# Performance work log

Measured on AMD Instinct MI355X. Metric: run time of the kernel, lower is better.

Reference implementation:

```python
import math
import jax, jax.numpy as jnp
import numpy as np

N, DIN, DOUT = 32768, 1024, 1024
C = 1.0            # ball curvature c (k = -c)
MIN_NORM = 1e-15
EPS_PROJ = 4e-3    # geoopt float32 boundary eps


def _safe_norm(x):
    # sqrt of clipped sum-of-squares: finite value and finite grad at 0
    return jnp.sqrt(jnp.clip(jnp.sum(x * x, axis=-1, keepdims=True), MIN_NORM))


def _artanh(u):
    return jnp.arctanh(jnp.clip(u, -1.0 + 1e-5, 1.0 - 1e-5))


def _project(x, c):
    norm = _safe_norm(x)
    maxnorm = (1.0 - EPS_PROJ) / jnp.sqrt(c)
    return jnp.where(norm > maxnorm, x / norm * maxnorm, x)


def _mobius_matvec(W, x, c):
    sqc = jnp.sqrt(c)
    x_norm = _safe_norm(x)                       # [N,1]
    mx = x @ W.T                                 # [N,DOUT]
    mx_norm = _safe_norm(mx)                     # [N,1]
    res = jnp.tanh(mx_norm / x_norm * _artanh(sqc * x_norm)) * mx / (mx_norm * sqc)
    zero = jnp.all(mx == 0, axis=-1, keepdims=True)
    return jnp.where(zero, jnp.zeros((), x.dtype), res)


def _expmap0(u, c):
    sqc = jnp.sqrt(c)
    u_norm = _safe_norm(u)
    return jnp.tanh(sqc * u_norm) * u / (sqc * u_norm)


def _mobius_add(x, y, c):
    x2 = jnp.sum(x * x, axis=-1, keepdims=True)
    y2 = jnp.sum(y * y, axis=-1, keepdims=True)
    xy = jnp.sum(x * y, axis=-1, keepdims=True)
    num = (1.0 + 2.0 * c * xy + c * y2) * x + (1.0 - c * x2) * y
    denom = 1.0 + 2.0 * c * xy + c * c * x2 * y2
    return num / jnp.clip(denom, MIN_NORM)


def setup_inputs() -> dict:
    key = jax.random.key(0)
    kx, kw, kb = jax.random.split(key, 3)
    x = jax.random.normal(kx, (N, DIN), jnp.float32)
    # place points strictly inside the unit Poincare ball
    x = x / (jnp.linalg.norm(x, axis=-1, keepdims=True) + 1.0) * 0.7
    limit = math.sqrt(2.0) * math.sqrt(6.0 / (DIN + DOUT))  # xavier_uniform gain=sqrt(2)
    weight = jax.random.uniform(kw, (DOUT, DIN), jnp.float32, -limit, limit)
    bias = 0.01 * jax.random.normal(kb, (DOUT,), jnp.float32)
    return {"x": x, "weight": weight, "bias": bias}


def reference(x, weight, bias) -> jnp.ndarray:
    c = jnp.float32(C)
    res = _mobius_matvec(weight, x, c)           # dropout=0 / eval: weight used as-is
    res = _project(res, c)
    hyp_bias = _project(_expmap0(bias[None, :], c), c)
    res = _project(_mobius_add(res, hyp_bias, c), c)
    return res
```

## Files before the change

### kernel.cpp

```cpp
#include <hip/hip_runtime.h>
#include <hip/hip_bf16.h>
#include <cmath>

#define NROWS 32768
#define DIN   1024
#define DOUT  1024
#define BM    64
#define BK    32
#define NKT   (DIN / BK)
#define MAXNORM 0.996f
#define XPAD  40

typedef __attribute__((ext_vector_type(8))) __bf16 bf16x8;
typedef __attribute__((ext_vector_type(4))) float  f32x4;

__device__ __forceinline__ void gload16(const void* g, void* l) {
    __builtin_amdgcn_global_load_lds(
        (const __attribute__((address_space(1))) void*)g,
        (__attribute__((address_space(3))) void*)l, 16, 0, 0);
}

__device__ __forceinline__ unsigned pack2bf(float a, float b) {
    union { unsigned u; __bf16 h[2]; } p;
    p.h[0] = (__bf16)a; p.h[1] = (__bf16)b;
    return p.u;
}

#define WAITBAR(N) do {                                                   \
    asm volatile("s_waitcnt vmcnt(" #N ") lgkmcnt(0)" ::: "memory");      \
    __builtin_amdgcn_s_barrier();                                         \
    __builtin_amdgcn_sched_barrier(0);                                    \
} while (0)

__global__ void conv_w_kernel(const float* __restrict__ Wf, __bf16* __restrict__ Wb) {
    int cid = blockIdx.x * blockDim.x + threadIdx.x;
    int q  = cid & 3;
    int r  = (cid >> 2) & 15;
    int g2 = (cid >> 6) & 31;
    int h  = (cid >> 11) & 1;
    int kt = cid >> 12;
    int n  = ((g2 << 1) + h) * 16 + r;
    int k0 = kt * BK + ((q ^ ((r >> 1) & 3)) << 3);
    const float* src = Wf + (size_t)n * DIN + k0;
    f32x4 v0 = *(const f32x4*)src;
    f32x4 v1 = *(const f32x4*)(src + 4);
    uint4 o;
    o.x = pack2bf(v0[0], v0[1]); o.y = pack2bf(v0[2], v0[3]);
    o.z = pack2bf(v1[0], v1[1]); o.w = pack2bf(v1[2], v1[3]);
    *(uint4*)((char*)Wb + (size_t)cid * 16) = o;
}

__global__ __launch_bounds__(512, 2) void hyp_kernel_pipe(
    const float* __restrict__ X,
    const __bf16* __restrict__ Wb,
    const float* __restrict__ bias,
    float* __restrict__ out)
{
    __shared__ __align__(16) __bf16 WtA[2][512 * BK];
    __shared__ __align__(16) __bf16 WtB[2][512 * BK];
    __shared__ __align__(16) __bf16 Xt[2][BM * XPAD];
    __shared__ float hbs[DOUT];
    __shared__ float redq[BM][8];
    __shared__ float redd[BM][8];
    __shared__ float xsqs[BM];
    __shared__ float fco[BM][2];
    __shared__ float bred[8];

    const int tid  = threadIdx.x;
    const int lane = tid & 63;
    const int wid  = tid >> 6;
    const int l15  = lane & 15;
    const int l4   = lane >> 4;
    const int row0 = blockIdx.x * BM;

    const int xr = tid >> 3;
    const int xk = (tid & 7) * 4;
    const float* xp = X + (size_t)(row0 + xr) * DIN + xk;
    float xsq = 0.f;

    f32x4 acc[4][8];
    #pragma unroll
    for (int m = 0; m < 4; m++)
        #pragma unroll
        for (int nt = 0; nt < 8; nt++)
            acc[m][nt] = (f32x4){0.f, 0.f, 0.f, 0.f};

    auto wsrc = [&](int kt, int h) -> const char* {
        return (const char*)Wb + (((size_t)kt * 2 + h) << 15);
    };
    auto issueHalf = [&](const char* g, __bf16* lds) {
        #pragma unroll
        for (int j = 0; j < 4; j++) {
            int c = (j << 9) + tid;
            gload16(g + (size_t)c * 16,
                    (char*)lds + (((j << 9) + (wid << 6)) << 4));
        }
    };

    f32x4 xv;
    auto xload  = [&](int kt) { xv = *(const f32x4*)(xp + kt * BK); };
    auto xstage = [&](int dstbuf) {
        xsq += xv[0]*xv[0] + xv[1]*xv[1] + xv[2]*xv[2] + xv[3]*xv[3];
        uint2 pk;
        pk.x = pack2bf(xv[0], xv[1]);
        pk.y = pack2bf(xv[2], xv[3]);
        *(uint2*)((char*)(&Xt[dstbuf][0]) + xr * (XPAD * 2) + xk * 2) = pk;
    };

    bf16x8 afr[4];
    auto cmpA = [&](int buf) {
        const char* xb = (const char*)(&Xt[buf][0]);
        const char* wb = (const char*)(&WtA[buf][0]);
        #pragma unroll
        for (int m = 0; m < 4; m++)
            afr[m] = *(const bf16x8*)(xb + ((m << 4) + l15) * (XPAD * 2) + (l4 << 4));
        bf16x8 b[4];
        #pragma unroll
        for (int i = 0; i < 4; i++) {
            int g2 = (wid << 2) + i;
            b[i] = *(const bf16x8*)(wb + (((g2 << 6) + (l15 << 2) + (l4 ^ ((l15 >> 1) & 3))) << 4));
        }
        __builtin_amdgcn_s_setprio(1);
        #pragma unroll
        for (int i = 0; i < 4; i++)
            #pragma unroll
            for (int m = 0; m < 4; m++)
                acc[m][i * 2] = __builtin_amdgcn_mfma_f32_16x16x32_bf16(afr[m], b[i], acc[m][i * 2], 0, 0, 0);
        __builtin_amdgcn_s_setprio(0);
    };
    auto cmpB = [&](int buf) {
        const char* wb = (const char*)(&WtB[buf][0]);
        bf16x8 b[4];
        #pragma unroll
        for (int i = 0; i < 4; i++) {
            int g2 = (wid << 2) + i;
            b[i] = *(const bf16x8*)(wb + (((g2 << 6) + (l15 << 2) + (l4 ^ ((l15 >> 1) & 3))) << 4));
        }
        __builtin_amdgcn_s_setprio(1);
        #pragma unroll
        for (int i = 0; i < 4; i++)
            #pragma unroll
            for (int m = 0; m < 4; m++)
                acc[m][i * 2 + 1] = __builtin_amdgcn_mfma_f32_16x16x32_bf16(afr[m], b[i], acc[m][i * 2 + 1], 0, 0, 0);
        __builtin_amdgcn_s_setprio(0);
    };

    issueHalf(wsrc(0, 0), &WtA[0][0]);
    issueHalf(wsrc(0, 1), &WtB[0][0]);
    xload(0);

    float b0 = bias[tid], b1 = bias[tid + 512];
    float bs = b0 * b0 + b1 * b1;
    #pragma unroll
    for (int m = 1; m < 64; m <<= 1) bs += __shfl_xor(bs, m);
    if (lane == 0) bred[wid] = bs;
    __syncthreads();
    float tot = 0.f;
    #pragma unroll
    for (int i = 0; i < 8; i++) tot += bred[i];
    const float bnorm = sqrtf(fmaxf(tot, 1e-15f));
    const float bth   = tanhf(bnorm);
    float sc0 = bth / bnorm;
    float hn  = bth;
    if (hn > MAXNORM) { sc0 *= MAXNORM / hn; hn = MAXNORM; }
    hbs[tid]       = sc0 * b0;
    hbs[tid + 512] = sc0 * b1;
    const float y2c = hn * hn;
    __syncthreads();

    float hv[8];
    #pragma unroll
    for (int nt = 0; nt < 8; nt++) hv[nt] = hbs[(wid << 7) + (nt << 4) + l15];

    xstage(0);
    xload(1);

    for (int kt = 0; kt < 30; kt += 2) {
        issueHalf(wsrc(kt + 1, 0), &WtA[1][0]); WAITBAR(9); cmpA(0);
        xstage(1); xload(kt + 2);
        issueHalf(wsrc(kt + 1, 1), &WtB[1][0]); WAITBAR(9); cmpB(0);

        issueHalf(wsrc(kt + 2, 0), &WtA[0][0]); WAITBAR(9); cmpA(1);
        xstage(0); xload(kt + 3);
        issueHalf(wsrc(kt + 2, 1), &WtB[0][0]); WAITBAR(9); cmpB(1);
    }
    issueHalf(wsrc(31, 0), &WtA[1][0]); WAITBAR(9); cmpA(0);
    xstage(1);
    issueHalf(wsrc(31, 1), &WtB[1][0]); WAITBAR(8); cmpB(0);
    WAITBAR(4); cmpA(1);
    WAITBAR(0); cmpB(1);

    float xs = xsq;
    #pragma unroll
    for (int m = 1; m < 8; m <<= 1) xs += __shfl_xor(xs, m);
    if ((tid & 7) == 0) xsqs[xr] = xs;

    #pragma unroll
    for (int m = 0; m < 4; m++) {
        #pragma unroll
        for (int r = 0; r < 4; r++) {
            float s = 0.f, d = 0.f;
            #pragma unroll
            for (int nt = 0; nt < 8; nt++) {
                float v = acc[m][nt][r];
                s += v * v;
                d += v * hv[nt];
            }
            #pragma unroll
            for (int mm = 1; mm < 16; mm <<= 1) {
                s += __shfl_xor(s, mm);
                d += __shfl_xor(d, mm);
            }
            if (l15 == 0) {
                int rl = (m << 4) + (l4 << 2) + r;
                redq[rl][wid] = s;
                redd[rl][wid] = d;
            }
        }
    }
    __syncthreads();

    if (tid < BM) {
        int r = tid;
        float sq = 0.f, dt = 0.f;
        #pragma unroll
        for (int w = 0; w < 8; w++) { sq += redq[r][w]; dt += redd[r][w]; }
        float sx     = xsqs[r];
        float xnorm  = sqrtf(fmaxf(sx, 1e-15f));
        float mxnorm = sqrtf(fmaxf(sq, 1e-15f));
        float u  = fminf(xnorm, 1.f - 1e-5f);
        float tv = tanhf(mxnorm / xnorm * atanhf(u));
        float rn = fminf(tv, MAXNORM);
        float s  = rn / mxnorm;
        float xy = s * dt;
        float x2 = rn * rn;
        float Am = 1.f + 2.f * xy + y2c;
        float Bm = 1.f - x2;
        float Dm = fmaxf(1.f + 2.f * xy + x2 * y2c, 1e-15f);
        float g1 = Am * s / Dm;
        float g2 = Bm / Dm;
        float osq   = g1 * g1 * sq + 2.f * g1 * g2 * dt + g2 * g2 * y2c;
        float onorm = sqrtf(fmaxf(osq, 1e-15f));
        float psc   = onorm > MAXNORM ? MAXNORM / onorm : 1.f;
        fco[r][0] = g1 * psc;
        fco[r][1] = g2 * psc;
    }
    __syncthreads();

    #pragma unroll
    for (int m = 0; m < 4; m++) {
        #pragma unroll
        for (int r = 0; r < 4; r++) {
            int rl = (m << 4) + (l4 << 2) + r;
            float F1 = fco[rl][0], F2 = fco[rl][1];
            float* orow = out + (size_t)(row0 + rl) * DOUT + (wid << 7);
            #pragma unroll
            for (int nt = 0; nt < 8; nt++)
                orow[(nt << 4) + l15] = F1 * acc[m][nt][r] + F2 * hv[nt];
        }
    }
}

__global__ __launch_bounds__(512, 2) void hyp_kernel_basic(
    const float* __restrict__ X,
    const float* __restrict__ Wf,
    const float* __restrict__ bias,
    float* __restrict__ out)
{
    __shared__ __align__(16) __bf16 Wt[2][DOUT * BK];
    __shared__ __align__(16) __bf16 Xt[2][BM * XPAD];
    __shared__ float hbs[DOUT];
    __shared__ float redq[BM][8];
    __shared__ float redd[BM][8];
    __shared__ float xsqs[BM];
    __shared__ float fco[BM][2];
    __shared__ float bred[8];

    const int tid  = threadIdx.x;
    const int lane = tid & 63;
    const int wid  = tid >> 6;
    const int l15  = lane & 15;
    const int l4   = lane >> 4;
    const int row0 = blockIdx.x * BM;
    const int xr = tid >> 3;
    const int xk = (tid & 7) * 4;
    const float* xp = X + (size_t)(row0 + xr) * DIN + xk;
    float xsq = 0.f;

    f32x4 acc[4][8];
    #pragma unroll
    for (int m = 0; m < 4; m++)
        #pragma unroll
        for (int nt = 0; nt < 8; nt++)
            acc[m][nt] = (f32x4){0.f, 0.f, 0.f, 0.f};

    auto STAGE = [&](int buf, int kt) {
        if (kt < NKT) {
            #pragma unroll
            for (int j = 0; j < 8; j++) {
                int c = (j << 9) + tid;
                int q = c & 3, n = c >> 2;
                int k0 = kt * BK + ((q ^ ((n >> 1) & 3)) << 3);
                const float* src = Wf + (size_t)n * DIN + k0;
                f32x4 v0 = *(const f32x4*)src;
                f32x4 v1 = *(const f32x4*)(src + 4);
                uint4 o;
                o.x = pack2bf(v0[0], v0[1]); o.y = pack2bf(v0[2], v0[3]);
                o.z = pack2bf(v1[0], v1[1]); o.w = pack2bf(v1[2], v1[3]);
                *(uint4*)((char*)(&Wt[buf][0]) + c * 16) = o;
            }
            f32x4 xv = *(const f32x4*)(xp + kt * BK);
            xsq += xv[0]*xv[0] + xv[1]*xv[1] + xv[2]*xv[2] + xv[3]*xv[3];
            uint2 pk;
            pk.x = pack2bf(xv[0], xv[1]);
            pk.y = pack2bf(xv[2], xv[3]);
            *(uint2*)((char*)(&Xt[buf][0]) + xr * (XPAD * 2) + xk * 2) = pk;
        }
    };

    STAGE(0, 0);

    float b0 = bias[tid], b1 = bias[tid + 512];
    float bs = b0 * b0 + b1 * b1;
    #pragma unroll
    for (int m = 1; m < 64; m <<= 1) bs += __shfl_xor(bs, m);
    if (lane == 0) bred[wid] = bs;
    __syncthreads();
    float tot = 0.f;
    #pragma unroll
    for (int i = 0; i < 8; i++) tot += bred[i];
    const float bnorm = sqrtf(fmaxf(tot, 1e-15f));
    const float bth   = tanhf(bnorm);
    float sc0 = bth / bnorm;
    float hn  = bth;
    if (hn > MAXNORM) { sc0 *= MAXNORM / hn; hn = MAXNORM; }
    hbs[tid]       = sc0 * b0;
    hbs[tid + 512] = sc0 * b1;
    const float y2c = hn * hn;
    __syncthreads();

    float hv[8];
    #pragma unroll
    for (int nt = 0; nt < 8; nt++) hv[nt] = hbs[(wid << 7) + (nt << 4) + l15];

    int cur = 0;
    for (int kt = 0; kt < NKT; kt++) {
        STAGE(cur ^ 1, kt + 1);
        const char* xb = (const char*)(&Xt[cur][0]);
        const char* wb = (const char*)(&Wt[cur][0]);
        bf16x8 a[4], b[8];
        #pragma unroll
        for (int m = 0; m < 4; m++)
            a[m] = *(const bf16x8*)(xb + ((m << 4) + l15) * (XPAD * 2) + (l4 << 4));
        #pragma unroll
        for (int nt = 0; nt < 8; nt++) {
            int n = (wid << 7) + (nt << 4) + l15;
            b[nt] = *(const bf16x8*)(wb + n * 64 + ((l4 ^ ((n >> 1) & 3)) << 4));
        }
        #pragma unroll
        for (int m = 0; m < 4; m++)
            #pragma unroll
            for (int nt = 0; nt < 8; nt++)
                acc[m][nt] = __builtin_amdgcn_mfma_f32_16x16x32_bf16(a[m], b[nt], acc[m][nt], 0, 0, 0);
        __syncthreads();
        cur ^= 1;
    }

    float xs = xsq;
    #pragma unroll
    for (int m = 1; m < 8; m <<= 1) xs += __shfl_xor(xs, m);
    if ((tid & 7) == 0) xsqs[xr] = xs;

    #pragma unroll
    for (int m = 0; m < 4; m++) {
        #pragma unroll
        for (int r = 0; r < 4; r++) {
            float s = 0.f, d = 0.f;
            #pragma unroll
            for (int nt = 0; nt < 8; nt++) {
                float v = acc[m][nt][r];
                s += v * v;
                d += v * hv[nt];
            }
            #pragma unroll
            for (int mm = 1; mm < 16; mm <<= 1) {
                s += __shfl_xor(s, mm);
                d += __shfl_xor(d, mm);
            }
            if (l15 == 0) {
                int rl = (m << 4) + (l4 << 2) + r;
                redq[rl][wid] = s;
                redd[rl][wid] = d;
            }
        }
    }
    __syncthreads();

    if (tid < BM) {
        int r = tid;
        float sq = 0.f, dt = 0.f;
        #pragma unroll
        for (int w = 0; w < 8; w++) { sq += redq[r][w]; dt += redd[r][w]; }
        float sx     = xsqs[r];
        float xnorm  = sqrtf(fmaxf(sx, 1e-15f));
        float mxnorm = sqrtf(fmaxf(sq, 1e-15f));
        float u  = fminf(xnorm, 1.f - 1e-5f);
        float tv = tanhf(mxnorm / xnorm * atanhf(u));
        float rn = fminf(tv, MAXNORM);
        float s  = rn / mxnorm;
        float xy = s * dt;
        float x2 = rn * rn;
        float Am = 1.f + 2.f * xy + y2c;
        float Bm = 1.f - x2;
        float Dm = fmaxf(1.f + 2.f * xy + x2 * y2c, 1e-15f);
        float g1 = Am * s / Dm;
        float g2 = Bm / Dm;
        float osq   = g1 * g1 * sq + 2.f * g1 * g2 * dt + g2 * g2 * y2c;
        float onorm = sqrtf(fmaxf(osq, 1e-15f));
        float psc   = onorm > MAXNORM ? MAXNORM / onorm : 1.f;
        fco[r][0] = g1 * psc;
        fco[r][1] = g2 * psc;
    }
    __syncthreads();

    #pragma unroll
    for (int m = 0; m < 4; m++) {
        #pragma unroll
        for (int r = 0; r < 4; r++) {
            int rl = (m << 4) + (l4 << 2) + r;
            float F1 = fco[rl][0], F2 = fco[rl][1];
            float* orow = out + (size_t)(row0 + rl) * DOUT + (wid << 7);
            #pragma unroll
            for (int nt = 0; nt < 8; nt++)
                orow[(nt << 4) + l15] = F1 * acc[m][nt][r] + F2 * hv[nt];
        }
    }
}

extern "C" void kernel_launch(void* const* d_in, const int* in_sizes, int n_in,
                              void* d_out, int out_size, void* d_ws, size_t ws_size,
                              hipStream_t stream) {
    const float* X    = (const float*)d_in[0];
    const float* W    = (const float*)d_in[1];
    const float* bias = (const float*)d_in[2];
    float* out = (float*)d_out;

    const size_t wb_bytes = (size_t)DOUT * DIN * 2;
    if (ws_size >= wb_bytes) {
        __bf16* Wb = (__bf16*)d_ws;
        conv_w_kernel<<<dim3(512), dim3(256), 0, stream>>>(W, Wb);
        hyp_kernel_pipe<<<dim3(NROWS / BM), dim3(512), 0, stream>>>(X, Wb, bias, out);
    } else {
        hyp_kernel_basic<<<dim3(NROWS / BM), dim3(512), 0, stream>>>(X, W, bias, out);
    }
}
```

Before: 121.7 us.

## Load weight fragments directly into registers from pre-laid-out global buffer

Replaces the LDS-staged async weight pipeline with a 1024-thread kernel where each wave loads its bf16 weight MFMA fragments straight from global memory into registers, prefetched one k-step ahead, and only X goes through a triple-buffered LDS tile. The weight conversion kernel is rewritten to emit a fragment-major layout so each lane's loads are contiguous. This drops the LDS traffic and bank pressure for W and frees shared memory. In exchange, every wave re-reads W from L2 with only a one-step prefetch, so global latency may be exposed. Per-wave output width shrinks from 128 to 64 columns, which lowers reuse of the X fragments.

After: 112.1 us. 7.8% less time.

```diff
diff --git a/kernel.cpp b/kernel.cpp
--- a/kernel.cpp
+++ b/kernel.cpp
@@ -14,50 +14,213 @@
 typedef __attribute__((ext_vector_type(8))) __bf16 bf16x8;
 typedef __attribute__((ext_vector_type(4))) float  f32x4;
 
-__device__ __forceinline__ void gload16(const void* g, void* l) {
-    __builtin_amdgcn_global_load_lds(
-        (const __attribute__((address_space(1))) void*)g,
-        (__attribute__((address_space(3))) void*)l, 16, 0, 0);
-}
-
 __device__ __forceinline__ unsigned pack2bf(float a, float b) {
     union { unsigned u; __bf16 h[2]; } p;
     p.h[0] = (__bf16)a; p.h[1] = (__bf16)b;
     return p.u;
 }
 
-#define WAITBAR(N) do {                                                   \
-    asm volatile("s_waitcnt vmcnt(" #N ") lgkmcnt(0)" ::: "memory");      \
-    __builtin_amdgcn_s_barrier();                                         \
-    __builtin_amdgcn_sched_barrier(0);                                    \
-} while (0)
-
 __global__ void conv_w_kernel(const float* __restrict__ Wf, __bf16* __restrict__ Wb) {
-    int cid = blockIdx.x * blockDim.x + threadIdx.x;
-    int q  = cid & 3;
-    int r  = (cid >> 2) & 15;
-    int g2 = (cid >> 6) & 31;
-    int h  = (cid >> 11) & 1;
-    int kt = cid >> 12;
-    int n  = ((g2 << 1) + h) * 16 + r;
-    int k0 = kt * BK + ((q ^ ((r >> 1) & 3)) << 3);
+    int c  = blockIdx.x * blockDim.x + threadIdx.x;
+    int l  = c & 63;
+    int j  = (c >> 6) & 63;
+    int kt = c >> 12;
+    int n  = j * 16 + (l & 15);
+    int k0 = kt * 32 + (l >> 4) * 8;
     const float* src = Wf + (size_t)n * DIN + k0;
     f32x4 v0 = *(const f32x4*)src;
     f32x4 v1 = *(const f32x4*)(src + 4);
     uint4 o;
     o.x = pack2bf(v0[0], v0[1]); o.y = pack2bf(v0[2], v0[3]);
     o.z = pack2bf(v1[0], v1[1]); o.w = pack2bf(v1[2], v1[3]);
-    *(uint4*)((char*)Wb + (size_t)cid * 16) = o;
+    *(uint4*)((char*)Wb + (size_t)c * 16) = o;
 }
 
-__global__ __launch_bounds__(512, 2) void hyp_kernel_pipe(
+__global__ __launch_bounds__(1024) void hyp_kernel_reg(
     const float* __restrict__ X,
     const __bf16* __restrict__ Wb,
     const float* __restrict__ bias,
     float* __restrict__ out)
 {
-    __shared__ __align__(16) __bf16 WtA[2][512 * BK];
-    __shared__ __align__(16) __bf16 WtB[2][512 * BK];
+    __shared__ __align__(16) __bf16 Xt[3][BM * XPAD];
+    __shared__ float hbs[DOUT];
+    __shared__ float xsqs[BM];
+    __shared__ float fco[BM][2];
+    __shared__ float bred[16];
+
+    const int tid  = threadIdx.x;
+    const int lane = tid & 63;
+    const int wid  = tid >> 6;
+    const int l15  = lane & 15;
+    const int l4   = lane >> 4;
+    const int row0 = blockIdx.x * BM;
+
+    const int xr = tid >> 4;
+    const int xk = (tid & 15) * 2;
+    const float* xp = X + (size_t)(row0 + xr) * DIN + xk;
+    float xsq = 0.f;
+
+    const __bf16* wp = Wb + ((size_t)(wid * 4) * 64 + lane) * 8;
+
+    f32x4 acc[4][4];
+    #pragma unroll
+    for (int m = 0; m < 4; m++)
+        #pragma unroll
+        for (int n = 0; n < 4; n++)
+            acc[m][n] = (f32x4){0.f, 0.f, 0.f, 0.f};
+
+    float2 xw = *(const float2*)xp;
+    float2 xf = *(const float2*)(xp + BK);
+    bf16x8 bfr[4];
+    #pragma unroll
+    for (int i = 0; i < 4; i++) bfr[i] = *(const bf16x8*)(wp + i * 512);
+
+    float bv = bias[tid];
+    float bs = bv * bv;
+    #pragma unroll
+    for (int m = 1; m < 64; m <<= 1) bs += __shfl_xor(bs, m);
+    if (lane == 0) bred[wid] = bs;
+    __syncthreads();
+    float tot = 0.f;
+    #pragma unroll
+    for (int i = 0; i < 16; i++) tot += bred[i];
+    const float bnorm = sqrtf(fmaxf(tot, 1e-15f));
+    const float bth   = tanhf(bnorm);
+    float sc0 = bth / bnorm;
+    float hn  = bth;
+    if (hn > MAXNORM) { sc0 *= MAXNORM / hn; hn = MAXNORM; }
+    hbs[tid] = sc0 * bv;
+    const float y2c = hn * hn;
+
+    xsq += xw.x * xw.x + xw.y * xw.y;
+    *(unsigned*)((char*)(&Xt[0][0]) + xr * (XPAD * 2) + xk * 2) = pack2bf(xw.x, xw.y);
+    xw = xf;
+    xf = *(const float2*)(xp + 2 * BK);
+
+    int br = 0, bw = 1;
+    for (int kt = 0; kt < NKT; kt++) {
+        if (kt + 1 < NKT) {
+            xsq += xw.x * xw.x + xw.y * xw.y;
+            *(unsigned*)((char*)(&Xt[bw][0]) + xr * (XPAD * 2) + xk * 2) = pack2bf(xw.x, xw.y);
+        }
+        xw = xf;
+        int xt = kt + 3 < NKT ? kt + 3 : NKT - 1;
+        xf = *(const float2*)(xp + (size_t)xt * BK);
+
+        asm volatile("s_waitcnt lgkmcnt(0)" ::: "memory");
+        __builtin_amdgcn_s_barrier();
+        __builtin_amdgcn_sched_barrier(0);
+
+        bf16x8 a[4];
+        const char* xb = (const char*)(&Xt[br][0]);
+        #pragma unroll
+        for (int m = 0; m < 4; m++)
+            a[m] = *(const bf16x8*)(xb + ((m << 4) + l15) * (XPAD * 2) + (l4 << 4));
+
+        __builtin_amdgcn_s_setprio(1);
+        #pragma unroll
+        for (int n = 0; n < 4; n++)
+            #pragma unroll
+            for (int m = 0; m < 4; m++)
+                acc[m][n] = __builtin_amdgcn_mfma_f32_16x16x32_bf16(a[m], bfr[n], acc[m][n], 0, 0, 0);
+        __builtin_amdgcn_s_setprio(0);
+
+        int ktb = kt + 1 < NKT ? kt + 1 : NKT - 1;
+        const __bf16* wkp = wp + (size_t)ktb * 32768;
+        #pragma unroll
+        for (int i = 0; i < 4; i++) bfr[i] = *(const bf16x8*)(wkp + i * 512);
+
+        br = br + 1 == 3 ? 0 : br + 1;
+        bw = bw + 1 == 3 ? 0 : bw + 1;
+    }
+
+    __syncthreads();
+
+    float* redq = (float*)(&Xt[0][0]);
+    float* redd = redq + BM * 16;
+
+    float xs = xsq;
+    #pragma unroll
+    for (int m = 1; m < 16; m <<= 1) xs += __shfl_xor(xs, m);
+    if (l15 == 0) xsqs[xr] = xs;
+
+    float hv[4];
+    #pragma unroll
+    for (int n = 0; n < 4; n++) hv[n] = hbs[(wid << 6) + (n << 4) + l15];
+
+    #pragma unroll
+    for (int m = 0; m < 4; m++) {
+        #pragma unroll
+        for (int r = 0; r < 4; r++) {
+            float s = 0.f, d = 0.f;
+            #pragma unroll
+            for (int n = 0; n < 4; n++) {
+                float v = acc[m][n][r];
+                s += v * v;
+                d += v * hv[n];
+            }
+            #pragma unroll
+            for (int mm = 1; mm < 16; mm <<= 1) {
+                s += __shfl_xor(s, mm);
+                d += __shfl_xor(d, mm);
+            }
+            if (l15 == 0) {
+                int rl = (m << 4) + (l4 << 2) + r;
+                redq[rl * 16 + wid] = s;
+                redd[rl * 16 + wid] = d;
+            }
+        }
+    }
+    __syncthreads();
+
+    if (tid < BM) {
+        int r = tid;
+        float sq = 0.f, dt = 0.f;
+        #pragma unroll
+        for (int w = 0; w < 16; w++) { sq += redq[r * 16 + w]; dt += redd[r * 16 + w]; }
+        float sx     = xsqs[r];
+        float xnorm  = sqrtf(fmaxf(sx, 1e-15f));
+        float mxnorm = sqrtf(fmaxf(sq, 1e-15f));
+        float u  = fminf(xnorm, 1.f - 1e-5f);
+        float tv = tanhf(mxnorm / xnorm * atanhf(u));
+        float rn = fminf(tv, MAXNORM);
+        float s  = rn / mxnorm;
+        float xy = s * dt;
+        float x2 = rn * rn;
+        float Am = 1.f + 2.f * xy + y2c;
+        float Bm = 1.f - x2;
+        float Dm = fmaxf(1.f + 2.f * xy + x2 * y2c, 1e-15f);
+        float g1 = Am * s / Dm;
+        float g2 = Bm / Dm;
+        float osq   = g1 * g1 * sq + 2.f * g1 * g2 * dt + g2 * g2 * y2c;
+        float onorm = sqrtf(fmaxf(osq, 1e-15f));
+        float psc   = onorm > MAXNORM ? MAXNORM / onorm : 1.f;
+        fco[r][0] = g1 * psc;
+        fco[r][1] = g2 * psc;
+    }
+    __syncthreads();
+
+    #pragma unroll
+    for (int m = 0; m < 4; m++) {
+        #pragma unroll
+        for (int r = 0; r < 4; r++) {
+            int rl = (m << 4) + (l4 << 2) + r;
+            float F1 = fco[rl][0], F2 = fco[rl][1];
+            float* orow = out + (size_t)(row0 + rl) * DOUT + (wid << 6);
+            #pragma unroll
+            for (int n = 0; n < 4; n++)
+                orow[(n << 4) + l15] = F1 * acc[m][n][r] + F2 * hv[n];
+        }
+    }
+}
+
+__global__ __launch_bounds__(512, 2) void hyp_kernel_basic(
+    const float* __restrict__ X,
+    const float* __restrict__ Wf,
+    const float* __restrict__ bias,
+    float* __restrict__ out)
+{
+    __shared__ __align__(16) __bf16 Wt[2][DOUT * BK];
     __shared__ __align__(16) __bf16 Xt[2][BM * XPAD];
     __shared__ float hbs[DOUT];
     __shared__ float redq[BM][8];
@@ -72,7 +235,6 @@
     const int l15  = lane & 15;
     const int l4   = lane >> 4;
     const int row0 = blockIdx.x * BM;
-
     const int xr = tid >> 3;
     const int xk = (tid & 7) * 4;
     const float* xp = X + (size_t)(row0 + xr) * DIN + xk;
@@ -85,69 +247,31 @@
         for (int nt = 0; nt < 8; nt++)
             acc[m][nt] = (f32x4){0.f, 0.f, 0.f, 0.f};
 
-    auto wsrc = [&](int kt, int h) -> const char* {
-        return (const char*)Wb + (((size_t)kt * 2 + h) << 15);
+    auto STAGE = [&](int buf, int kt) {
+        if (kt < NKT) {
+            #pragma unroll
+            for (int j = 0; j < 8; j++) {
+                int c = (j << 9) + tid;
+                int q = c & 3, n = c >> 2;
+                int k0 = kt * BK + ((q ^ ((n >> 1) & 3)) << 3);
+                const float* src = Wf + (size_t)n * DIN + k0;
+                f32x4 v0 = *(const f32x4*)src;
+                f32x4 v1 = *(const f32x4*)(src + 4);
+                uint4 o;
+                o.x = pack2bf(v0[0], v0[1]); o.y = pack2bf(v0[2], v0[3]);
+                o.z = pack2bf(v1[0], v1[1]); o.w = pack2bf(v1[2], v1[3]);
+                *(uint4*)((char*)(&Wt[buf][0]) + c * 16) = o;
+            }
+            f32x4 xv = *(const f32x4*)(xp + kt * BK);
+            xsq += xv[0]*xv[0] + xv[1]*xv[1] + xv[2]*xv[2] + xv[3]*xv[3];
+            uint2 pk;
+            pk.x = pack2bf(xv[0], xv[1]);
+            pk.y = pack2bf(xv[2], xv[3]);
+            *(uint2*)((char*)(&Xt[buf][0]) + xr * (XPAD * 2) + xk * 2) = pk;
+        }
     };
-    auto issueHalf = [&](const char* g, __bf16* lds) {
-        #pragma unroll
-        for (int j = 0; j < 4; j++) {
-            int c = (j << 9) + tid;
-            gload16(g + (size_t)c * 16,
-                    (char*)lds + (((j << 9) + (wid << 6)) << 4));
-        }
-    };
-
-    f32x4 xv;
-    auto xload  = [&](int kt) { xv = *(const f32x4*)(xp + kt * BK); };
-    auto xstage = [&](int dstbuf) {
-        xsq += xv[0]*xv[0] + xv[1]*xv[1] + xv[2]*xv[2] + xv[3]*xv[3];
-        uint2 pk;
-        pk.x = pack2bf(xv[0], xv[1]);
-        pk.y = pack2bf(xv[2], xv[3]);
-        *(uint2*)((char*)(&Xt[dstbuf][0]) + xr * (XPAD * 2) + xk * 2) = pk;
-    };
-
-    bf16x8 afr[4];
-    auto cmpA = [&](int buf) {
-        const char* xb = (const char*)(&Xt[buf][0]);
-        const char* wb = (const char*)(&WtA[buf][0]);
-        #pragma unroll
-        for (int m = 0; m < 4; m++)
-            afr[m] = *(const bf16x8*)(xb + ((m << 4) + l15) * (XPAD * 2) + (l4 << 4));
-        bf16x8 b[4];
-        #pragma unroll
-        for (int i = 0; i < 4; i++) {
-            int g2 = (wid << 2) + i;
-            b[i] = *(const bf16x8*)(wb + (((g2 << 6) + (l15 << 2) + (l4 ^ ((l15 >> 1) & 3))) << 4));
-        }
-        __builtin_amdgcn_s_setprio(1);
-        #pragma unroll
-        for (int i = 0; i < 4; i++)
-            #pragma unroll
-            for (int m = 0; m < 4; m++)
-                acc[m][i * 2] = __builtin_amdgcn_mfma_f32_16x16x32_bf16(afr[m], b[i], acc[m][i * 2], 0, 0, 0);
-        __builtin_amdgcn_s_setprio(0);
-    };
-    auto cmpB = [&](int buf) {
-        const char* wb = (const char*)(&WtB[buf][0]);
-        bf16x8 b[4];
-        #pragma unroll
-        for (int i = 0; i < 4; i++) {
-            int g2 = (wid << 2) + i;
-            b[i] = *(const bf16x8*)(wb + (((g2 << 6) + (l15 << 2) + (l4 ^ ((l15 >> 1) & 3))) << 4));
-        }
-        __builtin_amdgcn_s_setprio(1);
-        #pragma unroll
-        for (int i = 0; i < 4; i++)
-            #pragma unroll
-            for (int m = 0; m < 4; m++)
-                acc[m][i * 2 + 1] = __builtin_amdgcn_mfma_f32_16x16x32_bf16(afr[m], b[i], acc[m][i * 2 + 1], 0, 0, 0);
-        __builtin_amdgcn_s_setprio(0);
-    };
-
-    issueHalf(wsrc(0, 0), &WtA[0][0]);
-    issueHalf(wsrc(0, 1), &WtB[0][0]);
-    xload(0);
+
+    STAGE(0, 0);
 
     float b0 = bias[tid], b1 = bias[tid + 512];
     float bs = b0 * b0 + b1 * b1;
@@ -172,23 +296,28 @@
     #pragma unroll
     for (int nt = 0; nt < 8; nt++) hv[nt] = hbs[(wid << 7) + (nt << 4) + l15];
 
-    xstage(0);
-    xload(1);
-
-    for (int kt = 0; kt < 30; kt += 2) {
-        issueHalf(wsrc(kt + 1, 0), &WtA[1][0]); WAITBAR(9); cmpA(0);
-        xstage(1); xload(kt + 2);
-        issueHalf(wsrc(kt + 1, 1), &WtB[1][0]); WAITBAR(9); cmpB(0);
-
-        issueHalf(wsrc(kt + 2, 0), &WtA[0][0]); WAITBAR(9); cmpA(1);
-        xstage(0); xload(kt + 3);
-        issueHalf(wsrc(kt + 2, 1), &WtB[0][0]); WAITBAR(9); cmpB(1);
-    }
-    issueHalf(wsrc(31, 0), &WtA[1][0]); WAITBAR(9); cmpA(0);
-    xstage(1);
-    issueHalf(wsrc(31, 1), &WtB[1][0]); WAITBAR(8); cmpB(0);
-    WAITBAR(4); cmpA(1);
-    WAITBAR(0); cmpB(1);
+    int cur = 0;
+    for (int kt = 0; kt < NKT; kt++) {
+        STAGE(cur ^ 1, kt + 1);
+        const char* xb = (const char*)(&Xt[cur][0]);
+        const char* wb = (const char*)(&Wt[cur][0]);
+        bf16x8 a[4], b[8];
+        #pragma unroll
+        for (int m = 0; m < 4; m++)
+            a[m] = *(const bf16x8*)(xb + ((m << 4) + l15) * (XPAD * 2) + (l4 << 4));
+        #pragma unroll
+        for (int nt = 0; nt < 8; nt++) {
+            int n = (wid << 7) + (nt << 4) + l15;
+            b[nt] = *(const bf16x8*)(wb + n * 64 + ((l4 ^ ((n >> 1) & 3)) << 4));
+        }
+        #pragma unroll
+        for (int m = 0; m < 4; m++)
+            #pragma unroll
+            for (int nt = 0; nt < 8; nt++)
+                acc[m][nt] = __builtin_amdgcn_mfma_f32_16x16x32_bf16(a[m], b[nt], acc[m][nt], 0, 0, 0);
+        __syncthreads();
+        cur ^= 1;
+    }
 
     float xs = xsq;
     #pragma unroll
@@ -261,182 +390,6 @@
     }
 }
 
-__global__ __launch_bounds__(512, 2) void hyp_kernel_basic(
-    const float* __restrict__ X,
-    const float* __restrict__ Wf,
-    const float* __restrict__ bias,
-    float* __restrict__ out)
-{
-    __shared__ __align__(16) __bf16 Wt[2][DOUT * BK];
-    __shared__ __align__(16) __bf16 Xt[2][BM * XPAD];
-    __shared__ float hbs[DOUT];
-    __shared__ float redq[BM][8];
-    __shared__ float redd[BM][8];
-    __shared__ float xsqs[BM];
-    __shared__ float fco[BM][2];
-    __shared__ float bred[8];
-
-    const int tid  = threadIdx.x;
-    const int lane = tid & 63;
-    const int wid  = tid >> 6;
-    const int l15  = lane & 15;
-    const int l4   = lane >> 4;
-    const int row0 = blockIdx.x * BM;
-    const int xr = tid >> 3;
-    const int xk = (tid & 7) * 4;
-    const float* xp = X + (size_t)(row0 + xr) * DIN + xk;
-    float xsq = 0.f;
-
-    f32x4 acc[4][8];
-    #pragma unroll
-    for (int m = 0; m < 4; m++)
-        #pragma unroll
-        for (int nt = 0; nt < 8; nt++)
-            acc[m][nt] = (f32x4){0.f, 0.f, 0.f, 0.f};
-
-    auto STAGE = [&](int buf, int kt) {
-        if (kt < NKT) {
-            #pragma unroll
-            for (int j = 0; j < 8; j++) {
-                int c = (j << 9) + tid;
-                int q = c & 3, n = c >> 2;
-                int k0 = kt * BK + ((q ^ ((n >> 1) & 3)) << 3);
-                const float* src = Wf + (size_t)n * DIN + k0;
-                f32x4 v0 = *(const f32x4*)src;
-                f32x4 v1 = *(const f32x4*)(src + 4);
-                uint4 o;
-                o.x = pack2bf(v0[0], v0[1]); o.y = pack2bf(v0[2], v0[3]);
-                o.z = pack2bf(v1[0], v1[1]); o.w = pack2bf(v1[2], v1[3]);
-                *(uint4*)((char*)(&Wt[buf][0]) + c * 16) = o;
-            }
-            f32x4 xv = *(const f32x4*)(xp + kt * BK);
-            xsq += xv[0]*xv[0] + xv[1]*xv[1] + xv[2]*xv[2] + xv[3]*xv[3];
-            uint2 pk;
-            pk.x = pack2bf(xv[0], xv[1]);
-            pk.y = pack2bf(xv[2], xv[3]);
-            *(uint2*)((char*)(&Xt[buf][0]) + xr * (XPAD * 2) + xk * 2) = pk;
-        }
-    };
-
-    STAGE(0, 0);
-
-    float b0 = bias[tid], b1 = bias[tid + 512];
-    float bs = b0 * b0 + b1 * b1;
-    #pragma unroll
-    for (int m = 1; m < 64; m <<= 1) bs += __shfl_xor(bs, m);
-    if (lane == 0) bred[wid] = bs;
-    __syncthreads();
-    float tot = 0.f;
-    #pragma unroll
-    for (int i = 0; i < 8; i++) tot += bred[i];
-    const float bnorm = sqrtf(fmaxf(tot, 1e-15f));
-    const float bth   = tanhf(bnorm);
-    float sc0 = bth / bnorm;
-    float hn  = bth;
-    if (hn > MAXNORM) { sc0 *= MAXNORM / hn; hn = MAXNORM; }
-    hbs[tid]       = sc0 * b0;
-    hbs[tid + 512] = sc0 * b1;
-    const float y2c = hn * hn;
-    __syncthreads();
-
-    float hv[8];
-    #pragma unroll
-    for (int nt = 0; nt < 8; nt++) hv[nt] = hbs[(wid << 7) + (nt << 4) + l15];
-
-    int cur = 0;
-    for (int kt = 0; kt < NKT; kt++) {
-        STAGE(cur ^ 1, kt + 1);
-        const char* xb = (const char*)(&Xt[cur][0]);
-        const char* wb = (const char*)(&Wt[cur][0]);
-        bf16x8 a[4], b[8];
-        #pragma unroll
-        for (int m = 0; m < 4; m++)
-            a[m] = *(const bf16x8*)(xb + ((m << 4) + l15) * (XPAD * 2) + (l4 << 4));
-        #pragma unroll
-        for (int nt = 0; nt < 8; nt++) {
-            int n = (wid << 7) + (nt << 4) + l15;
-            b[nt] = *(const bf16x8*)(wb + n * 64 + ((l4 ^ ((n >> 1) & 3)) << 4));
-        }
-        #pragma unroll
-        for (int m = 0; m < 4; m++)
-            #pragma unroll
-            for (int nt = 0; nt < 8; nt++)
-                acc[m][nt] = __builtin_amdgcn_mfma_f32_16x16x32_bf16(a[m], b[nt], acc[m][nt], 0, 0, 0);
-        __syncthreads();
-        cur ^= 1;
-    }
-
-    float xs = xsq;
-    #pragma unroll
-    for (int m = 1; m < 8; m <<= 1) xs += __shfl_xor(xs, m);
-    if ((tid & 7) == 0) xsqs[xr] = xs;
-
-    #pragma unroll
-    for (int m = 0; m < 4; m++) {
-        #pragma unroll
-        for (int r = 0; r < 4; r++) {
-            float s = 0.f, d = 0.f;
-            #pragma unroll
-            for (int nt = 0; nt < 8; nt++) {
-                float v = acc[m][nt][r];
-                s += v * v;
-                d += v * hv[nt];
-            }
-            #pragma unroll
-            for (int mm = 1; mm < 16; mm <<= 1) {
-                s += __shfl_xor(s, mm);
-                d += __shfl_xor(d, mm);
-            }
-            if (l15 == 0) {
-                int rl = (m << 4) + (l4 << 2) + r;
-                redq[rl][wid] = s;
-                redd[rl][wid] = d;
-            }
-        }
-    }
-    __syncthreads();
-
-    if (tid < BM) {
-        int r = tid;
-        float sq = 0.f, dt = 0.f;
-        #pragma unroll
-        for (int w = 0; w < 8; w++) { sq += redq[r][w]; dt += redd[r][w]; }
-        float sx     = xsqs[r];
-        float xnorm  = sqrtf(fmaxf(sx, 1e-15f));
-        float mxnorm = sqrtf(fmaxf(sq, 1e-15f));
-        float u  = fminf(xnorm, 1.f - 1e-5f);
-        float tv = tanhf(mxnorm / xnorm * atanhf(u));
-        float rn = fminf(tv, MAXNORM);
-        float s  = rn / mxnorm;
-        float xy = s * dt;
-        float x2 = rn * rn;
-        float Am = 1.f + 2.f * xy + y2c;
-        float Bm = 1.f - x2;
-        float Dm = fmaxf(1.f + 2.f * xy + x2 * y2c, 1e-15f);
-        float g1 = Am * s / Dm;
-        float g2 = Bm / Dm;
-        float osq   = g1 * g1 * sq + 2.f * g1 * g2 * dt + g2 * g2 * y2c;
-        float onorm = sqrtf(fmaxf(osq, 1e-15f));
-        float psc   = onorm > MAXNORM ? MAXNORM / onorm : 1.f;
-        fco[r][0] = g1 * psc;
-        fco[r][1] = g2 * psc;
-    }
-    __syncthreads();
-
-    #pragma unroll
-    for (int m = 0; m < 4; m++) {
-        #pragma unroll
-        for (int r = 0; r < 4; r++) {
-            int rl = (m << 4) + (l4 << 2) + r;
-            float F1 = fco[rl][0], F2 = fco[rl][1];
-            float* orow = out + (size_t)(row0 + rl) * DOUT + (wid << 7);
-            #pragma unroll
-            for (int nt = 0; nt < 8; nt++)
-                orow[(nt << 4) + l15] = F1 * acc[m][nt][r] + F2 * hv[nt];
-        }
-    }
-}
-
 extern "C" void kernel_launch(void* const* d_in, const int* in_sizes, int n_in,
                               void* d_out, int out_size, void* d_ws, size_t ws_size,
                               hipStream_t stream) {
@@ -449,7 +402,7 @@
     if (ws_size >= wb_bytes) {
         __bf16* Wb = (__bf16*)d_ws;
         conv_w_kernel<<<dim3(512), dim3(256), 0, stream>>>(W, Wb);
-        hyp_kernel_pipe<<<dim3(NROWS / BM), dim3(512), 0, stream>>>(X, Wb, bias, out);
+        hyp_kernel_reg<<<dim3(NROWS / BM), dim3(1024), 0, stream>>>(X, Wb, bias, out);
     } else {
         hyp_kernel_basic<<<dim3(NROWS / BM), dim3(512), 0, stream>>>(X, W, bias, out);
     }
```
